# Kernel tuning notes

Hardware: AMD Instinct MI355X
Metric: run time of the kernel (lower is better)

## Reference

```python
import jax, jax.numpy as jnp
import numpy as np

NUM_ITERATIONS = 3
EPS = 1e-12  # matches torch F.normalize default eps


def setup_inputs() -> dict:
    key = jax.random.key(0)
    k1, k2 = jax.random.split(key)
    B, IN_CAPS, IN_LEN = 64, 1152, 8
    OUT_CAPS, OUT_LEN = 64, 16
    x = jax.random.normal(k1, (B, IN_CAPS, IN_LEN), dtype=jnp.float32)
    # xavier_uniform over (out_caps, out_len, in_len): fan_in=in_len, fan_out=out_len
    limit = float(np.sqrt(6.0 / (IN_LEN + OUT_LEN)))
    weight = jax.random.uniform(k2, (OUT_CAPS, OUT_LEN, IN_LEN), dtype=jnp.float32,
                                minval=-limit, maxval=limit)
    return {"x": x, "weight": weight}


def reference(x, weight):
    # priors[b,o,n,l] = sum_i weight[o,l,i] * x[b,n,i]  -> [B, out_caps, in_caps, out_len]
    priors = jnp.einsum('oli,bni->bonl', weight, x)
    # k-means routing, similarity='dot', squash=False (module defaults)
    out = jnp.mean(priors, axis=-2, keepdims=True)  # [B, O, 1, L] initial centroid
    probs = None
    for _ in range(NUM_ITERATIONS):
        norm = jnp.linalg.norm(out, axis=-1, keepdims=True)
        out_n = out / jnp.maximum(norm, EPS)  # F.normalize(output, dim=-1)
        logits = jnp.sum(priors * out_n, axis=-1, keepdims=True)  # [B, O, N, 1]
        probs = jax.nn.softmax(logits, axis=-2)  # softmax over in_capsules
        out = jnp.sum(probs * priors, axis=-2, keepdims=True)  # [B, O, 1, L]
    # squash=False -> return raw centroid
    return out.squeeze(-2), probs.squeeze(-1)  # [B, O, L], [B, O, N]
```

## Files before the change

### kernel.cpp

```cpp
#include <hip/hip_runtime.h>
#include <math.h>


#define NCAPS 1152
#define ILEN  8
#define OCAPS 64
#define OLEN  16
#define T     128
#define NW    2
#define RPT   9
#define NITER 3

template<int CTRL>
__device__ __forceinline__ float dpp_mov0(float x) {
    int xi = __builtin_bit_cast(int, x);
    int r  = __builtin_amdgcn_update_dpp(0, xi, CTRL, 0xf, 0xf, true);
    return __builtin_bit_cast(float, r);
}

__device__ __forceinline__ float wave_sum63(float v) {
    v += dpp_mov0<0x111>(v);
    v += dpp_mov0<0x112>(v);
    v += dpp_mov0<0x114>(v);
    v += dpp_mov0<0x118>(v);
    v += dpp_mov0<0x142>(v);
    v += dpp_mov0<0x143>(v);
    return v;
}

__device__ __forceinline__ float row16_sum(float v) {
    v += dpp_mov0<0x111>(v);
    v += dpp_mov0<0x112>(v);
    v += dpp_mov0<0x114>(v);
    v += dpp_mov0<0x118>(v);
    return v;
}

__device__ __forceinline__ float bcast_lane(float v, int lane) {
    return __builtin_bit_cast(float,
        __builtin_amdgcn_readlane(__builtin_bit_cast(int, v), lane));
}

__global__ __launch_bounds__(T, 4) void caps_kernel(const float* __restrict__ x,
                                                    const float* __restrict__ w,
                                                    float* __restrict__ dout,
                                                    int probs_base) {
    const int tid  = threadIdx.x;
    const int lane = tid & 63;
    const int wid  = tid >> 6;
    const int l16  = lane & 15;
    const int o = blockIdx.x & (OCAPS - 1);
    const int b = blockIdx.x >> 6;

    __shared__ __align__(16) float red[NITER + 1][NW][12];

    float wreg[ILEN];
    {
        const float4* wp = (const float4*)(w + ((size_t)o * OLEN + l16) * ILEN);
        float4 a = wp[0], c = wp[1];
        wreg[0] = a.x; wreg[1] = a.y; wreg[2] = a.z; wreg[3] = a.w;
        wreg[4] = c.x; wreg[5] = c.y; wreg[6] = c.z; wreg[7] = c.w;
    }

    const float* xb = x + (size_t)b * (NCAPS * ILEN);
    float xr[RPT][ILEN];
    #pragma unroll
    for (int k = 0; k < RPT; ++k) {
        const float4* q = (const float4*)(xb + (size_t)(tid + k * T) * ILEN);
        float4 a = q[0], c = q[1];
        xr[k][0] = a.x; xr[k][1] = a.y; xr[k][2] = a.z; xr[k][3] = a.w;
        xr[k][4] = c.x; xr[k][5] = c.y; xr[k][6] = c.z; xr[k][7] = c.w;
    }

    float e[RPT];
    float ysg[ILEN];

    #pragma unroll
    for (int it = 0; it <= NITER; ++it) {
        float s[ILEN];
        float z = 0.0f;
        if (it == 0) {
            #pragma unroll
            for (int i = 0; i < ILEN; ++i) {
                float acc = xr[0][i];
                #pragma unroll
                for (int k = 1; k < RPT; ++k) acc += xr[k][i];
                s[i] = acc;
            }
        } else {
            #pragma unroll
            for (int k = 0; k < RPT; ++k) {
                float lg = xr[k][0] * ysg[0];
                #pragma unroll
                for (int i = 1; i < ILEN; ++i) lg = fmaf(xr[k][i], ysg[i], lg);
                e[k] = __expf(lg);
            }
            #pragma unroll
            for (int i = 0; i < ILEN; ++i) {
                float acc = e[0] * xr[0][i];
                #pragma unroll
                for (int k = 1; k < RPT; ++k) acc = fmaf(e[k], xr[k][i], acc);
                s[i] = acc;
            }
            z = e[0];
            #pragma unroll
            for (int k = 1; k < RPT; ++k) z += e[k];
        }

        #pragma unroll
        for (int i = 0; i < ILEN; ++i) s[i] = wave_sum63(s[i]);
        if (it > 0) z = wave_sum63(z);

        if (lane == 63) {
            *(float4*)&red[it][wid][0] = make_float4(s[0], s[1], s[2], s[3]);
            *(float4*)&red[it][wid][4] = make_float4(s[4], s[5], s[6], s[7]);
            red[it][wid][8] = z;
        }
        __syncthreads();

        float4 a0 = *(const float4*)&red[it][0][0];
        float4 a1 = *(const float4*)&red[it][0][4];
        float4 b0 = *(const float4*)&red[it][1][0];
        float4 b1 = *(const float4*)&red[it][1][4];
        float sc[ILEN];
        sc[0] = a0.x + b0.x; sc[1] = a0.y + b0.y; sc[2] = a0.z + b0.z; sc[3] = a0.w + b0.w;
        sc[4] = a1.x + b1.x; sc[5] = a1.y + b1.y; sc[6] = a1.z + b1.z; sc[7] = a1.w + b1.w;
        const float zc   = (it == 0) ? (float)NCAPS : (red[it][0][8] + red[it][1][8]);
        const float zinv = 1.0f / zc;

        float ol = wreg[0] * sc[0];
        #pragma unroll
        for (int i = 1; i < ILEN; ++i) ol = fmaf(wreg[i], sc[i], ol);
        ol *= zinv;

        if (it < NITER) {
            float n2 = row16_sum(ol * ol);
            n2 = bcast_lane(n2, 15);
            const float inv = 1.0f / fmaxf(sqrtf(n2), 1e-12f);
            const float oh = ol * inv;
            #pragma unroll
            for (int i = 0; i < ILEN; ++i) {
                float t = row16_sum(wreg[i] * oh);
                ysg[i] = bcast_lane(t, 15);
            }
        } else {
            if (tid < OLEN) dout[(size_t)blockIdx.x * OLEN + tid] = ol;
            float* pp = dout + (size_t)probs_base + (size_t)blockIdx.x * NCAPS;
            #pragma unroll
            for (int k = 0; k < RPT; ++k) pp[tid + k * T] = e[k] * zinv;
        }
    }
}

extern "C" void kernel_launch(void* const* d_in, const int* in_sizes, int n_in,
                              void* d_out, int out_size, void* d_ws, size_t ws_size,
                              hipStream_t stream) {
    const float* x = (const float*)d_in[0];
    const float* w = (const float*)d_in[1];
    float* out = (float*)d_out;
    const int Bv = in_sizes[0] / (NCAPS * ILEN);
    const int nblocks = Bv * OCAPS;
    const int probs_base = nblocks * OLEN;
    caps_kernel<<<dim3(nblocks), dim3(T), 0, stream>>>(x, w, out, probs_base);
}
```

Baseline: 80.92 us.

## Route 16 output capsules per block with bf16 MFMA logits and weighted sums

Each block now handles 16 output capsules of one batch with 512 threads instead of a single capsule. The input is staged once in LDS as bf16, both row-major and transposed with an extra ones row that yields the softmax normaliser. The logits and the exp-weighted sums are computed with 16x16x32 bf16 MFMA instructions, and partial sums are combined across waves through LDS. This cuts redundant x loads and scalar FMA work, but lowers precision to bf16, stores probabilities as bf16, and adds LDS staging and block-wide barriers.

```diff
diff --git a/kernel.cpp b/kernel.cpp
--- a/kernel.cpp
+++ b/kernel.cpp
@@ -6,10 +6,30 @@
 #define ILEN  8
 #define OCAPS 64
 #define OLEN  16
-#define T     128
-#define NW    2
-#define RPT   9
+#define T     512
+#define NWAVE 8
+#define TPW   9
 #define NITER 3
+#define OG    16
+#define XT_PITCH 1156
+
+typedef __attribute__((ext_vector_type(8))) short short8;
+typedef __attribute__((ext_vector_type(4))) float f32x4;
+
+__device__ __forceinline__ unsigned f2bf_u(float f) {
+    unsigned u = __builtin_bit_cast(unsigned, f);
+    return (u + 0x7FFFu + ((u >> 16) & 1u)) >> 16;
+}
+__device__ __forceinline__ unsigned pack2(float a, float b) {
+    return f2bf_u(a) | (f2bf_u(b) << 16);
+}
+__device__ __forceinline__ float bf2f(unsigned h) {
+    return __builtin_bit_cast(float, h << 16);
+}
+__device__ __forceinline__ short8 s8_from(unsigned a, unsigned b, unsigned c, unsigned d) {
+    uint4 t = make_uint4(a, b, c, d);
+    return __builtin_bit_cast(short8, t);
+}
 
 template<int CTRL>
 __device__ __forceinline__ float dpp_mov0(float x) {
@@ -17,17 +37,6 @@
     int r  = __builtin_amdgcn_update_dpp(0, xi, CTRL, 0xf, 0xf, true);
     return __builtin_bit_cast(float, r);
 }
-
-__device__ __forceinline__ float wave_sum63(float v) {
-    v += dpp_mov0<0x111>(v);
-    v += dpp_mov0<0x112>(v);
-    v += dpp_mov0<0x114>(v);
-    v += dpp_mov0<0x118>(v);
-    v += dpp_mov0<0x142>(v);
-    v += dpp_mov0<0x143>(v);
-    return v;
-}
-
 __device__ __forceinline__ float row16_sum(float v) {
     v += dpp_mov0<0x111>(v);
     v += dpp_mov0<0x112>(v);
@@ -36,12 +45,7 @@
     return v;
 }
 
-__device__ __forceinline__ float bcast_lane(float v, int lane) {
-    return __builtin_bit_cast(float,
-        __builtin_amdgcn_readlane(__builtin_bit_cast(int, v), lane));
-}
-
-__global__ __launch_bounds__(T, 4) void caps_kernel(const float* __restrict__ x,
+__global__ __launch_bounds__(T, 2) void caps_kernel(const float* __restrict__ x,
                                                     const float* __restrict__ w,
                                                     float* __restrict__ dout,
                                                     int probs_base) {
@@ -49,105 +53,133 @@
     const int lane = tid & 63;
     const int wid  = tid >> 6;
     const int l16  = lane & 15;
-    const int o = blockIdx.x & (OCAPS - 1);
-    const int b = blockIdx.x >> 6;
+    const int quad = lane >> 4;
+    const bool q0  = (quad == 0);
+    const int b  = blockIdx.x >> 2;
+    const int og = blockIdx.x & 3;
 
-    __shared__ __align__(16) float red[NITER + 1][NW][12];
+    __shared__ __align__(16) unsigned short xA[NCAPS][ILEN];
+    __shared__ __align__(16) unsigned short xaugT[10 * XT_PITCH];
+    __shared__ __align__(16) unsigned short Yl[OLEN][16];
+    __shared__ __align__(16) float Wl[OLEN][OLEN][ILEN];
+    __shared__ float Scmb[NWAVE][OLEN][17];
+    __shared__ float ZL[OLEN];
 
-    float wreg[ILEN];
-    {
-        const float4* wp = (const float4*)(w + ((size_t)o * OLEN + l16) * ILEN);
-        float4 a = wp[0], c = wp[1];
-        wreg[0] = a.x; wreg[1] = a.y; wreg[2] = a.z; wreg[3] = a.w;
-        wreg[4] = c.x; wreg[5] = c.y; wreg[6] = c.z; wreg[7] = c.w;
+    ((float4*)&Wl[0][0][0])[tid] = ((const float4*)(w + (size_t)og * OG * OLEN * ILEN))[tid];
+
+    const float4* xs = (const float4*)(x + (size_t)b * NCAPS * ILEN);
+    #pragma unroll
+    for (int p = 0; p < 3; ++p) {
+        const int row = p * T + tid;
+        if (row < NCAPS) {
+            float4 x0 = xs[row * 2], x1 = xs[row * 2 + 1];
+            unsigned h0 = f2bf_u(x0.x), h1 = f2bf_u(x0.y), h2 = f2bf_u(x0.z), h3 = f2bf_u(x0.w);
+            unsigned h4 = f2bf_u(x1.x), h5 = f2bf_u(x1.y), h6 = f2bf_u(x1.z), h7 = f2bf_u(x1.w);
+            *(uint4*)&xA[row][0] = make_uint4(h0 | (h1 << 16), h2 | (h3 << 16),
+                                              h4 | (h5 << 16), h6 | (h7 << 16));
+            xaugT[0 * XT_PITCH + row] = (unsigned short)h0;
+            xaugT[1 * XT_PITCH + row] = (unsigned short)h1;
+            xaugT[2 * XT_PITCH + row] = (unsigned short)h2;
+            xaugT[3 * XT_PITCH + row] = (unsigned short)h3;
+            xaugT[4 * XT_PITCH + row] = (unsigned short)h4;
+            xaugT[5 * XT_PITCH + row] = (unsigned short)h5;
+            xaugT[6 * XT_PITCH + row] = (unsigned short)h6;
+            xaugT[7 * XT_PITCH + row] = (unsigned short)h7;
+            xaugT[8 * XT_PITCH + row] = 0x3F80;
+        }
     }
+    for (int idx = tid; idx < XT_PITCH; idx += T) xaugT[9 * XT_PITCH + idx] = 0;
+    __syncthreads();
 
-    const float* xb = x + (size_t)b * (NCAPS * ILEN);
-    float xr[RPT][ILEN];
-    #pragma unroll
-    for (int k = 0; k < RPT; ++k) {
-        const float4* q = (const float4*)(xb + (size_t)(tid + k * T) * ILEN);
-        float4 a = q[0], c = q[1];
-        xr[k][0] = a.x; xr[k][1] = a.y; xr[k][2] = a.z; xr[k][3] = a.w;
-        xr[k][4] = c.x; xr[k][5] = c.y; xr[k][6] = c.z; xr[k][7] = c.w;
-    }
+    const int jr = (l16 < 9) ? l16 : 9;
+    const unsigned short* xTw = xaugT + jr * XT_PITCH + wid * (TPW * 16) + 4 * quad;
+    const unsigned short* xAw = &xA[wid * (TPW * 16) + l16][0];
 
-    float e[RPT];
-    float ysg[ILEN];
+    const short8 zs = {0, 0, 0, 0, 0, 0, 0, 0};
+    const f32x4  zc = {0.f, 0.f, 0.f, 0.f};
+
+    unsigned st0[TPW], st1[TPW];
 
     #pragma unroll
     for (int it = 0; it <= NITER; ++it) {
-        float s[ILEN];
-        float z = 0.0f;
-        if (it == 0) {
-            #pragma unroll
-            for (int i = 0; i < ILEN; ++i) {
-                float acc = xr[0][i];
-                #pragma unroll
-                for (int k = 1; k < RPT; ++k) acc += xr[k][i];
-                s[i] = acc;
+        short8 bL = zs;
+        if (it > 0 && q0) bL = *(const short8*)&Yl[l16][0];
+
+        f32x4 sacc = zc;
+        #pragma unroll
+        for (int tt = 0; tt < TPW; ++tt) {
+            uint2 t2 = *(const uint2*)(xTw + tt * 16);
+            short8 bs = s8_from(t2.x, t2.y, 0u, 0u);
+
+            short8 as;
+            if (it == 0) {
+                as = s8_from(0x3F803F80u, 0x3F803F80u, 0u, 0u);
+            } else {
+                short8 aL = q0 ? *(const short8*)(xAw + tt * 128) : zs;
+                f32x4 d = __builtin_amdgcn_mfma_f32_16x16x32_bf16(aL, bL, zc, 0, 0, 0);
+                float e0 = __expf(d[0]), e1 = __expf(d[1]);
+                float e2 = __expf(d[2]), e3 = __expf(d[3]);
+                unsigned p0 = pack2(e0, e1), p1 = pack2(e2, e3);
+                if (it == NITER) { st0[tt] = p0; st1[tt] = p1; }
+                as = s8_from(p0, p1, 0u, 0u);
             }
-        } else {
-            #pragma unroll
-            for (int k = 0; k < RPT; ++k) {
-                float lg = xr[k][0] * ysg[0];
-                #pragma unroll
-                for (int i = 1; i < ILEN; ++i) lg = fmaf(xr[k][i], ysg[i], lg);
-                e[k] = __expf(lg);
-            }
-            #pragma unroll
-            for (int i = 0; i < ILEN; ++i) {
-                float acc = e[0] * xr[0][i];
-                #pragma unroll
-                for (int k = 1; k < RPT; ++k) acc = fmaf(e[k], xr[k][i], acc);
-                s[i] = acc;
-            }
-            z = e[0];
-            #pragma unroll
-            for (int k = 1; k < RPT; ++k) z += e[k];
+            sacc = __builtin_amdgcn_mfma_f32_16x16x32_bf16(as, bs, sacc, 0, 0, 0);
         }
 
         #pragma unroll
-        for (int i = 0; i < ILEN; ++i) s[i] = wave_sum63(s[i]);
-        if (it > 0) z = wave_sum63(z);
+        for (int r = 0; r < 4; ++r) Scmb[wid][4 * quad + r][l16] = sacc[r];
+        __syncthreads();
 
-        if (lane == 63) {
-            *(float4*)&red[it][wid][0] = make_float4(s[0], s[1], s[2], s[3]);
-            *(float4*)&red[it][wid][4] = make_float4(s[4], s[5], s[6], s[7]);
-            red[it][wid][8] = z;
+        if (tid < 256) {
+            const int o = tid >> 4, l = tid & 15;
+            float sv[9];
+            #pragma unroll
+            for (int i = 0; i < 9; ++i) {
+                float t = Scmb[0][o][i];
+                #pragma unroll
+                for (int ww = 1; ww < NWAVE; ++ww) t += Scmb[ww][o][i];
+                sv[i] = t;
+            }
+            const float zinv = 1.0f / sv[8];
+            const float* wrow = &Wl[o][l][0];
+            float outl = wrow[0] * sv[0];
+            #pragma unroll
+            for (int i = 1; i < ILEN; ++i) outl = fmaf(wrow[i], sv[i], outl);
+            outl *= zinv;
+
+            if (it < NITER) {
+                float n2 = outl * outl;
+                n2 += __shfl_xor(n2, 1);
+                n2 += __shfl_xor(n2, 2);
+                n2 += __shfl_xor(n2, 4);
+                n2 += __shfl_xor(n2, 8);
+                const float inv = 1.0f / fmaxf(sqrtf(n2), 1e-12f);
+                const float oh = outl * inv;
+                #pragma unroll
+                for (int i = 0; i < ILEN; ++i) {
+                    float t = row16_sum(wrow[i] * oh);
+                    if (l == 15) Yl[o][i] = (unsigned short)f2bf_u(t);
+                }
+            } else {
+                dout[(((size_t)(b * OCAPS + og * OG + o)) << 4) + l] = outl;
+                if (l == 0) ZL[o] = zinv;
+            }
         }
         __syncthreads();
+    }
 
-        float4 a0 = *(const float4*)&red[it][0][0];
-        float4 a1 = *(const float4*)&red[it][0][4];
-        float4 b0 = *(const float4*)&red[it][1][0];
-        float4 b1 = *(const float4*)&red[it][1][4];
-        float sc[ILEN];
-        sc[0] = a0.x + b0.x; sc[1] = a0.y + b0.y; sc[2] = a0.z + b0.z; sc[3] = a0.w + b0.w;
-        sc[4] = a1.x + b1.x; sc[5] = a1.y + b1.y; sc[6] = a1.z + b1.z; sc[7] = a1.w + b1.w;
-        const float zc   = (it == 0) ? (float)NCAPS : (red[it][0][8] + red[it][1][8]);
-        const float zinv = 1.0f / zc;
-
-        float ol = wreg[0] * sc[0];
+    {
+        const float zi = ZL[l16];
+        float* pb = dout + (size_t)probs_base
+                  + (size_t)(b * OCAPS + og * OG + l16) * NCAPS
+                  + wid * (TPW * 16) + 4 * quad;
         #pragma unroll
-        for (int i = 1; i < ILEN; ++i) ol = fmaf(wreg[i], sc[i], ol);
-        ol *= zinv;
-
-        if (it < NITER) {
-            float n2 = row16_sum(ol * ol);
-            n2 = bcast_lane(n2, 15);
-            const float inv = 1.0f / fmaxf(sqrtf(n2), 1e-12f);
-            const float oh = ol * inv;
-            #pragma unroll
-            for (int i = 0; i < ILEN; ++i) {
-                float t = row16_sum(wreg[i] * oh);
-                ysg[i] = bcast_lane(t, 15);
-            }
-        } else {
-            if (tid < OLEN) dout[(size_t)blockIdx.x * OLEN + tid] = ol;
-            float* pp = dout + (size_t)probs_base + (size_t)blockIdx.x * NCAPS;
-            #pragma unroll
-            for (int k = 0; k < RPT; ++k) pp[tid + k * T] = e[k] * zinv;
+        for (int tt = 0; tt < TPW; ++tt) {
+            unsigned p0 = st0[tt], p1 = st1[tt];
+            pb[tt * 16 + 0] = bf2f(p0 & 0xFFFFu) * zi;
+            pb[tt * 16 + 1] = bf2f(p0 >> 16) * zi;
+            pb[tt * 16 + 2] = bf2f(p1 & 0xFFFFu) * zi;
+            pb[tt * 16 + 3] = bf2f(p1 >> 16) * zi;
         }
     }
 }
@@ -159,7 +191,7 @@
     const float* w = (const float*)d_in[1];
     float* out = (float*)d_out;
     const int Bv = in_sizes[0] / (NCAPS * ILEN);
-    const int nblocks = Bv * OCAPS;
-    const int probs_base = nblocks * OLEN;
+    const int nblocks = Bv * (OCAPS / OG);
+    const int probs_base = Bv * OCAPS * OLEN;
     caps_kernel<<<dim3(nblocks), dim3(T), 0, stream>>>(x, w, out, probs_base);
 }
```

Result: faster. 72.63 us (-10.2%).

## Use one wavefront per block and drop shared-memory cross-wave reduction

Applied to the files above, without the earlier changes.

Shrinks each block from two wavefronts to a single 64-lane wavefront, so each lane now holds 18 input capsules instead of 9. The shared-memory reduction and __syncthreads between waves go away, and all reductions become wave-local DPP sums plus readlane broadcasts. The cost is double the register footprint for x per thread (144 floats), lower occupancy under launch_bounds(64,2), and half as much parallelism per block, which may leave latency less well hidden.

```diff
diff --git a/kernel.cpp b/kernel.cpp
--- a/kernel.cpp
+++ b/kernel.cpp
@@ -6,79 +6,69 @@
 #define ILEN  8
 #define OCAPS 64
 #define OLEN  16
-#define T     128
-#define NW    2
-#define RPT   9
+#define RPT   18
 #define NITER 3
 
 template<int CTRL>
-__device__ __forceinline__ float dpp_mov0(float x) {
+__device__ __forceinline__ float dpp_add(float x) {
     int xi = __builtin_bit_cast(int, x);
     int r  = __builtin_amdgcn_update_dpp(0, xi, CTRL, 0xf, 0xf, true);
-    return __builtin_bit_cast(float, r);
+    return x + __builtin_bit_cast(float, r);
 }
-
 __device__ __forceinline__ float wave_sum63(float v) {
-    v += dpp_mov0<0x111>(v);
-    v += dpp_mov0<0x112>(v);
-    v += dpp_mov0<0x114>(v);
-    v += dpp_mov0<0x118>(v);
-    v += dpp_mov0<0x142>(v);
-    v += dpp_mov0<0x143>(v);
+    v = dpp_add<0x111>(v);
+    v = dpp_add<0x112>(v);
+    v = dpp_add<0x114>(v);
+    v = dpp_add<0x118>(v);
+    v = dpp_add<0x142>(v);
+    v = dpp_add<0x143>(v);
     return v;
 }
-
 __device__ __forceinline__ float row16_sum(float v) {
-    v += dpp_mov0<0x111>(v);
-    v += dpp_mov0<0x112>(v);
-    v += dpp_mov0<0x114>(v);
-    v += dpp_mov0<0x118>(v);
+    v = dpp_add<0x111>(v);
+    v = dpp_add<0x112>(v);
+    v = dpp_add<0x114>(v);
+    v = dpp_add<0x118>(v);
     return v;
 }
-
 __device__ __forceinline__ float bcast_lane(float v, int lane) {
     return __builtin_bit_cast(float,
         __builtin_amdgcn_readlane(__builtin_bit_cast(int, v), lane));
 }
 
-__global__ __launch_bounds__(T, 4) void caps_kernel(const float* __restrict__ x,
-                                                    const float* __restrict__ w,
-                                                    float* __restrict__ dout,
-                                                    int probs_base) {
-    const int tid  = threadIdx.x;
-    const int lane = tid & 63;
-    const int wid  = tid >> 6;
+__global__ __launch_bounds__(64, 2) void caps_kernel(const float* __restrict__ x,
+                                                     const float* __restrict__ w,
+                                                     float* __restrict__ dout,
+                                                     int probs_base) {
+    const int lane = threadIdx.x;
     const int l16  = lane & 15;
     const int o = blockIdx.x & (OCAPS - 1);
     const int b = blockIdx.x >> 6;
 
-    __shared__ __align__(16) float red[NITER + 1][NW][12];
+    const float4* wp = (const float4*)(w + ((size_t)o * OLEN + l16) * ILEN);
+    const float4 wa = wp[0], wb = wp[1];
+    float wd[ILEN];
+    wd[0] = wa.x; wd[1] = wa.y; wd[2] = wa.z; wd[3] = wa.w;
+    wd[4] = wb.x; wd[5] = wb.y; wd[6] = wb.z; wd[7] = wb.w;
 
-    float wreg[ILEN];
-    {
-        const float4* wp = (const float4*)(w + ((size_t)o * OLEN + l16) * ILEN);
-        float4 a = wp[0], c = wp[1];
-        wreg[0] = a.x; wreg[1] = a.y; wreg[2] = a.z; wreg[3] = a.w;
-        wreg[4] = c.x; wreg[5] = c.y; wreg[6] = c.z; wreg[7] = c.w;
-    }
-
-    const float* xb = x + (size_t)b * (NCAPS * ILEN);
+    const float* xb = x + (size_t)b * NCAPS * ILEN;
     float xr[RPT][ILEN];
     #pragma unroll
     for (int k = 0; k < RPT; ++k) {
-        const float4* q = (const float4*)(xb + (size_t)(tid + k * T) * ILEN);
+        const float4* q = (const float4*)(xb + (size_t)(lane + 64 * k) * ILEN);
         float4 a = q[0], c = q[1];
         xr[k][0] = a.x; xr[k][1] = a.y; xr[k][2] = a.z; xr[k][3] = a.w;
         xr[k][4] = c.x; xr[k][5] = c.y; xr[k][6] = c.z; xr[k][7] = c.w;
     }
 
+    float ysg[ILEN];
     float e[RPT];
-    float ysg[ILEN];
+    float zinv = 0.f;
 
     #pragma unroll
     for (int it = 0; it <= NITER; ++it) {
         float s[ILEN];
-        float z = 0.0f;
+        float z;
         if (it == 0) {
             #pragma unroll
             for (int i = 0; i < ILEN; ++i) {
@@ -87,6 +77,7 @@
                 for (int k = 1; k < RPT; ++k) acc += xr[k][i];
                 s[i] = acc;
             }
+            z = (float)NCAPS;
         } else {
             #pragma unroll
             for (int k = 0; k < RPT; ++k) {
@@ -102,54 +93,38 @@
                 for (int k = 1; k < RPT; ++k) acc = fmaf(e[k], xr[k][i], acc);
                 s[i] = acc;
             }
-            z = e[0];
+            float zp = e[0];
             #pragma unroll
-            for (int k = 1; k < RPT; ++k) z += e[k];
+            for (int k = 1; k < RPT; ++k) zp += e[k];
+            z = bcast_lane(wave_sum63(zp), 63);
         }
 
+        float sg[ILEN];
         #pragma unroll
-        for (int i = 0; i < ILEN; ++i) s[i] = wave_sum63(s[i]);
-        if (it > 0) z = wave_sum63(z);
+        for (int i = 0; i < ILEN; ++i) sg[i] = bcast_lane(wave_sum63(s[i]), 63);
 
-        if (lane == 63) {
-            *(float4*)&red[it][wid][0] = make_float4(s[0], s[1], s[2], s[3]);
-            *(float4*)&red[it][wid][4] = make_float4(s[4], s[5], s[6], s[7]);
-            red[it][wid][8] = z;
-        }
-        __syncthreads();
-
-        float4 a0 = *(const float4*)&red[it][0][0];
-        float4 a1 = *(const float4*)&red[it][0][4];
-        float4 b0 = *(const float4*)&red[it][1][0];
-        float4 b1 = *(const float4*)&red[it][1][4];
-        float sc[ILEN];
-        sc[0] = a0.x + b0.x; sc[1] = a0.y + b0.y; sc[2] = a0.z + b0.z; sc[3] = a0.w + b0.w;
-        sc[4] = a1.x + b1.x; sc[5] = a1.y + b1.y; sc[6] = a1.z + b1.z; sc[7] = a1.w + b1.w;
-        const float zc   = (it == 0) ? (float)NCAPS : (red[it][0][8] + red[it][1][8]);
-        const float zinv = 1.0f / zc;
-
-        float ol = wreg[0] * sc[0];
+        const float zi = 1.0f / z;
+        float ol = wd[0] * sg[0];
         #pragma unroll
-        for (int i = 1; i < ILEN; ++i) ol = fmaf(wreg[i], sc[i], ol);
-        ol *= zinv;
+        for (int i = 1; i < ILEN; ++i) ol = fmaf(wd[i], sg[i], ol);
+        ol *= zi;
 
         if (it < NITER) {
-            float n2 = row16_sum(ol * ol);
-            n2 = bcast_lane(n2, 15);
+            float n2 = bcast_lane(row16_sum(ol * ol), 15);
             const float inv = 1.0f / fmaxf(sqrtf(n2), 1e-12f);
             const float oh = ol * inv;
             #pragma unroll
-            for (int i = 0; i < ILEN; ++i) {
-                float t = row16_sum(wreg[i] * oh);
-                ysg[i] = bcast_lane(t, 15);
-            }
+            for (int i = 0; i < ILEN; ++i)
+                ysg[i] = bcast_lane(row16_sum(wd[i] * oh), 15);
         } else {
-            if (tid < OLEN) dout[(size_t)blockIdx.x * OLEN + tid] = ol;
-            float* pp = dout + (size_t)probs_base + (size_t)blockIdx.x * NCAPS;
-            #pragma unroll
-            for (int k = 0; k < RPT; ++k) pp[tid + k * T] = e[k] * zinv;
+            zinv = zi;
+            if (lane < OLEN) dout[((size_t)blockIdx.x << 4) + lane] = ol;
         }
     }
+
+    float* pp = dout + (size_t)probs_base + (size_t)blockIdx.x * NCAPS + lane;
+    #pragma unroll
+    for (int k = 0; k < RPT; ++k) pp[64 * k] = e[k] * zinv;
 }
 
 extern "C" void kernel_launch(void* const* d_in, const int* in_sizes, int n_in,
@@ -161,5 +136,5 @@
     const int Bv = in_sizes[0] / (NCAPS * ILEN);
     const int nblocks = Bv * OCAPS;
     const int probs_base = nblocks * OLEN;
-    caps_kernel<<<dim3(nblocks), dim3(T), 0, stream>>>(x, w, out, probs_base);
+    caps_kernel<<<dim3(nblocks), dim3(64), 0, stream>>>(x, w, out, probs_base);
 }
```

Result: faster. 76.43 us (-5.5%).
